# Performance work log

Hardware: AMD Instinct MI355X
Metric: run time of the kernel (lower is better)

The kernel has to match this reference:

```python
import jax, jax.numpy as jnp
import numpy as np

N = 50000
E = 800000
D_IN = 128
D_HID = 256


def setup_inputs() -> dict:
    key = jax.random.key(0)
    ks = jax.random.split(key, 9)
    x = jax.random.normal(ks[0], (N, D_IN), dtype=jnp.float32)
    edge_index = jax.random.randint(ks[1], (2, E), 0, N, dtype=jnp.int64)
    edge_weight = jax.random.uniform(ks[2], (E,), dtype=jnp.float32)
    # GCNConv params (lin: y = x @ W.T, plus bias added after aggregation)
    W1 = jax.random.normal(ks[3], (D_HID, D_IN), dtype=jnp.float32) / np.sqrt(D_IN)
    b1 = jnp.zeros((D_HID,), dtype=jnp.float32)
    W2 = jax.random.normal(ks[4], (D_IN, D_HID), dtype=jnp.float32) / np.sqrt(D_HID)
    b2 = jnp.zeros((D_IN,), dtype=jnp.float32)
    gamma = jnp.ones((D_IN,), dtype=jnp.float32)
    beta = jnp.zeros((D_IN,), dtype=jnp.float32)
    return {"x": x, "edge_index": edge_index, "edge_weight": edge_weight,
            "W1": W1, "b1": b1, "W2": W2, "b2": b2,
            "gamma": gamma, "beta": beta}


def _gcn_norm(edge_index, edge_weight, n_nodes):
    # add self loops with weight 1.0 (PyG gcn_norm default)
    loop = jnp.arange(n_nodes, dtype=edge_index.dtype)
    src = jnp.concatenate([edge_index[0], loop])
    dst = jnp.concatenate([edge_index[1], loop])
    w = jnp.concatenate([edge_weight, jnp.ones((n_nodes,), edge_weight.dtype)])
    # symmetric normalization: deg over target index
    deg = jax.ops.segment_sum(w, dst, num_segments=n_nodes)
    dinv = jnp.where(deg > 0, jax.lax.rsqrt(deg), 0.0)
    norm = dinv[src] * w * dinv[dst]
    return src, dst, norm


def _gcn_conv(x, src, dst, norm, W, b, n_nodes):
    h = x @ W.T                                    # [N, out]
    msg = h[src] * norm[:, None]                   # gather + scale [E+N, out]
    out = jax.ops.segment_sum(msg, dst, num_segments=n_nodes)
    return out + b


def reference(x, edge_index, edge_weight, W1, b1, W2, b2, gamma, beta):
    n_nodes = x.shape[0]
    src, dst, norm = _gcn_norm(edge_index, edge_weight, n_nodes)
    h = _gcn_conv(x, src, dst, norm, W1, b1, n_nodes)
    h = jax.nn.relu(h)
    h = _gcn_conv(h, src, dst, norm, W2, b2, n_nodes)
    # LayerNorm over last dim
    mu = jnp.mean(h, axis=-1, keepdims=True)
    var = jnp.mean(jnp.square(h - mu), axis=-1, keepdims=True)
    h = (h - mu) * jax.lax.rsqrt(var + 1e-5) * gamma + beta
    return h
```

## Files before the change

kernel.cpp:

```cpp
#include <hip/hip_runtime.h>

typedef unsigned short ushort_t;
typedef unsigned long long u64_t;
typedef __attribute__((ext_vector_type(8))) short short8;
typedef __attribute__((ext_vector_type(4))) float float4v;

__device__ inline float b2f(ushort_t u) {
    unsigned x = ((unsigned)u) << 16;
    return __builtin_bit_cast(float, x);
}
__device__ inline ushort_t f2b(float f) {
    unsigned x = __builtin_bit_cast(unsigned, f);
    unsigned r = (x + 0x7fffu + ((x >> 16) & 1u)) >> 16;
    return (ushort_t)r;
}


__global__ void k_mode(const int* __restrict__ ei, int E, int* mode) {
    __shared__ int any32;
    if (threadIdx.x == 0) any32 = 0;
    __syncthreads();
    for (int i = threadIdx.x; i < 1024; i += blockDim.x) {
        int slot = 2 * i + 1;
        if (slot < 2 * E && ei[slot] != 0) atomicOr(&any32, 1);
    }
    __syncthreads();
    if (threadIdx.x == 0) mode[0] = any32 ? 0 : 1;
}

__device__ inline int ld_src(const int* __restrict__ ei, int e, int E, int m64) {
    return m64 ? ei[2 * (size_t)e] : ei[e];
}
__device__ inline int ld_dst(const int* __restrict__ ei, int e, int E, int m64) {
    return m64 ? ei[2 * ((size_t)E + e)] : ei[(size_t)E + e];
}


__global__ void k_cast_x(const float* __restrict__ x, ushort_t* __restrict__ xb, int n4) {
    int i = blockIdx.x * blockDim.x + threadIdx.x;
    if (i >= n4) return;
    float4v v = ((const float4v*)x)[i];
    ushort4 o;
    o.x = f2b(v[0]); o.y = f2b(v[1]); o.z = f2b(v[2]); o.w = f2b(v[3]);
    ((ushort4*)xb)[i] = o;
}

__global__ void k_cast_w(const float* __restrict__ W1, const float* __restrict__ W2,
                         ushort_t* __restrict__ W1b, ushort_t* __restrict__ W2b) {
    int i = blockIdx.x * blockDim.x + threadIdx.x;
    if (i < 32768) W1b[i] = f2b(W1[i]);
    else W2b[i - 32768] = f2b(W2[i - 32768]);
}


__global__ void k_node_init(u64_t* packed, int Nn) {
    int i = blockIdx.x * blockDim.x + threadIdx.x;
    if (i < Nn) packed[i] = 0ull;
}

__global__ void k_count(const int* __restrict__ ei, const float* __restrict__ w,
                        const int* __restrict__ mode,
                        u64_t* packed, int* __restrict__ rank, int E, int Nn) {
    int e = blockIdx.x * blockDim.x + threadIdx.x;
    if (e >= E) return;
    int m64 = mode[0];
    int s = ld_src(ei, e, E, m64);
    int d = ld_dst(ei, e, E, m64);
    if ((unsigned)s < (unsigned)Nn && (unsigned)d < (unsigned)Nn) {
        unsigned fx = (unsigned)(w[e] * 16777216.0f + 0.5f);
        u64_t old = atomicAdd(packed + d, (1ull << 32) | (u64_t)fx);
        rank[e] = (int)(old >> 32);
    } else {
        rank[e] = -1;
    }
}

__device__ inline int cnt_hi(const u64_t* packed, int i) {
    return ((const int*)packed)[2 * i + 1];
}


__global__ __launch_bounds__(256) void k_scan_a(const u64_t* __restrict__ packed,
                                                int* __restrict__ bsum, int Nn) {
    int b = blockIdx.x, t = threadIdx.x;
    int base = b * 2048 + t * 8;
    int s = 0;
#pragma unroll
    for (int j = 0; j < 8; ++j) { int i = base + j; if (i < Nn) s += cnt_hi(packed, i); }
#pragma unroll
    for (int off = 1; off < 64; off <<= 1) s += __shfl_xor(s, off);
    __shared__ int wsum[4];
    if ((t & 63) == 0) wsum[t >> 6] = s;
    __syncthreads();
    if (t == 0) bsum[b] = wsum[0] + wsum[1] + wsum[2] + wsum[3];
}

__global__ void k_scan_b(const int* __restrict__ bsum, int* __restrict__ bbase,
                         int nb, int* __restrict__ offs, int Nn) {
    int t = threadIdx.x;
    int own = (t < nb) ? bsum[t] : 0;
    int v = own;
#pragma unroll
    for (int off = 1; off < 64; off <<= 1) {
        int u = __shfl_up(v, off);
        if (t >= off) v += u;
    }
    if (t < nb) bbase[t] = v - own;
    if (t == 63) offs[Nn] = v;
}

__global__ __launch_bounds__(256) void k_scan_c(const u64_t* __restrict__ packed,
                                                const int* __restrict__ bbase,
                                                int* __restrict__ offs, int Nn) {
    int b = blockIdx.x, t = threadIdx.x;
    int base = b * 2048 + t * 8;
    int v[8];
    int s = 0;
#pragma unroll
    for (int j = 0; j < 8; ++j) {
        int i = base + j;
        v[j] = (i < Nn) ? cnt_hi(packed, i) : 0;
        s += v[j];
    }
    __shared__ int sd[256];
    sd[t] = s;
    __syncthreads();
    for (int off = 1; off < 256; off <<= 1) {
        int u = (t >= off) ? sd[t - off] : 0;
        __syncthreads();
        sd[t] += u;
        __syncthreads();
    }
    int pos = bbase[b] + sd[t] - s;
#pragma unroll
    for (int j = 0; j < 8; ++j) {
        int i = base + j;
        if (i < Nn) { offs[i] = pos; pos += v[j]; }
    }
}

__global__ void k_dinv(const u64_t* __restrict__ packed, float* dinv, int Nn) {
    int i = blockIdx.x * blockDim.x + threadIdx.x;
    if (i >= Nn) return;
    float deg = 1.0f + (float)(unsigned)(packed[i] & 0xFFFFFFFFull) * (1.0f / 16777216.0f);
    dinv[i] = rsqrtf(deg);
}


__global__ void k_scatter(const int* __restrict__ ei, const float* __restrict__ w,
                          const int* __restrict__ mode,
                          const float* __restrict__ dinv,
                          const int* __restrict__ offs,
                          const int* __restrict__ rank,
                          int2* __restrict__ edata, int E, int Nn) {
    int e = blockIdx.x * blockDim.x + threadIdx.x;
    if (e >= E) return;
    int r = rank[e];
    if (r < 0) return;
    int m64 = mode[0];
    int s = ld_src(ei, e, E, m64);
    int d = ld_dst(ei, e, E, m64);
    int pos = offs[d] + r;
    float nw = dinv[s] * w[e] * dinv[d];
    int2 p;
    p.x = s;
    p.y = __builtin_bit_cast(int, nw);
    edata[pos] = p;
}


__device__ inline void agg_edges(const ushort_t* __restrict__ src,
                                 const int2* __restrict__ edata,
                                 int s, int e, int hl, int p, float* a) {
    int i = s;
    for (; i + 7 < e; i += 8) {
#pragma unroll
        for (int j = 0; j < 4; ++j) {
            int idx = i + p + 2 * j;
            int2 ed = edata[idx];
            float nw = __builtin_bit_cast(float, ed.y);
            ushort4 q = ((const ushort4*)(src + (size_t)ed.x * 128))[hl];
            a[0] += b2f(q.x) * nw; a[1] += b2f(q.y) * nw;
            a[2] += b2f(q.z) * nw; a[3] += b2f(q.w) * nw;
        }
    }
    for (; i < e; i += 2) {
        int idx = i + p;
        int ic = min(idx, e - 1);
        int2 ed = edata[ic];
        float nw = (idx < e) ? __builtin_bit_cast(float, ed.y) : 0.f;
        ushort4 q = ((const ushort4*)(src + (size_t)ed.x * 128))[hl];
        a[0] += b2f(q.x) * nw; a[1] += b2f(q.y) * nw;
        a[2] += b2f(q.z) * nw; a[3] += b2f(q.w) * nw;
    }
}

__global__ __launch_bounds__(256) void k_agg1(const ushort_t* __restrict__ xb,
                                              const int* __restrict__ offs,
                                              const int2* __restrict__ edata,
                                              const float* __restrict__ dinv,
                                              ushort_t* __restrict__ ax, int Nn) {
    int v = (blockIdx.x * blockDim.x + threadIdx.x) >> 6;
    int lane = threadIdx.x & 63;
    if (v >= Nn) return;
    int hl = lane & 31, p = lane >> 5;
    float a[4] = {0.f, 0.f, 0.f, 0.f};
    if (p == 0) {
        float dv = dinv[v];
        float sn = dv * dv;
        ushort4 pq = ((const ushort4*)(xb + (size_t)v * 128))[hl];
        a[0] = b2f(pq.x) * sn; a[1] = b2f(pq.y) * sn;
        a[2] = b2f(pq.z) * sn; a[3] = b2f(pq.w) * sn;
    }
    int s = offs[v], e = offs[v + 1];
    agg_edges(xb, edata, s, e, hl, p, a);
#pragma unroll
    for (int j = 0; j < 4; ++j) a[j] += __shfl_xor(a[j], 32);
    if (p == 0) {
        ushort4 o;
        o.x = f2b(a[0]); o.y = f2b(a[1]); o.z = f2b(a[2]); o.w = f2b(a[3]);
        ((ushort4*)(ax + (size_t)v * 128))[hl] = o;
    }
}


__global__ __launch_bounds__(256, 2) void k_gemm_fused(const ushort_t* __restrict__ ax,
                                                       const ushort_t* __restrict__ W1b,
                                                       const float* __restrict__ b1v,
                                                       const ushort_t* __restrict__ W2b,
                                                       ushort_t* __restrict__ h2, int Nn) {
    __shared__ ushort_t tile[64][264];
    int tid = threadIdx.x, wid = tid >> 6, lane = tid & 63;
    int m = lane & 15, q = lane >> 4;
    int blk = blockIdx.x * 64;

    short8 wf[4][4];
#pragma unroll
    for (int nt = 0; nt < 4; ++nt) {
        const ushort_t* wb = W1b + (size_t)(wid * 64 + nt * 16 + m) * 128 + q * 8;
#pragma unroll
        for (int kt = 0; kt < 4; ++kt) wf[nt][kt] = *(const short8*)(wb + kt * 32);
    }
    short8 af[4][4];
#pragma unroll
    for (int mi = 0; mi < 4; ++mi) {
        int arow = blk + mi * 16 + m;
        bool rv = arow < Nn;
        const ushort_t* ab = ax + (size_t)arow * 128 + q * 8;
#pragma unroll
        for (int kt = 0; kt < 4; ++kt)
            af[mi][kt] = rv ? *(const short8*)(ab + kt * 32) : (short8)0;
    }

    float4v acc1[4][4];
#pragma unroll
    for (int mi = 0; mi < 4; ++mi)
#pragma unroll
        for (int nt = 0; nt < 4; ++nt) acc1[mi][nt] = (float4v){0.f, 0.f, 0.f, 0.f};

#pragma unroll
    for (int kt = 0; kt < 4; ++kt)
#pragma unroll
        for (int mi = 0; mi < 4; ++mi)
#pragma unroll
            for (int nt = 0; nt < 4; ++nt)
                acc1[mi][nt] = __builtin_amdgcn_mfma_f32_16x16x32_bf16(
                    af[mi][kt], wf[nt][kt], acc1[mi][nt], 0, 0, 0);

#pragma unroll
    for (int nt = 0; nt < 4; ++nt) {
        int col = wid * 64 + nt * 16 + m;
        float bb = b1v[col];
#pragma unroll
        for (int mi = 0; mi < 4; ++mi) {
#pragma unroll
            for (int r = 0; r < 4; ++r) {
                float v = acc1[mi][nt][r] + bb;
                v = v > 0.f ? v : 0.f;
                tile[mi * 16 + q * 4 + r][col] = f2b(v);
            }
        }
    }
    __syncthreads();

    short8 w2f[2][8];
#pragma unroll
    for (int n2 = 0; n2 < 2; ++n2) {
        const ushort_t* wb = W2b + (size_t)(wid * 32 + n2 * 16 + m) * 256 + q * 8;
#pragma unroll
        for (int kt = 0; kt < 8; ++kt) w2f[n2][kt] = *(const short8*)(wb + kt * 32);
    }

    float4v acc2[4][2];
#pragma unroll
    for (int mi = 0; mi < 4; ++mi)
#pragma unroll
        for (int n2 = 0; n2 < 2; ++n2) acc2[mi][n2] = (float4v){0.f, 0.f, 0.f, 0.f};

#pragma unroll
    for (int kt = 0; kt < 8; ++kt) {
#pragma unroll
        for (int mi = 0; mi < 4; ++mi) {
            short8 a2 = *(const short8*)&tile[mi * 16 + m][kt * 32 + q * 8];
#pragma unroll
            for (int n2 = 0; n2 < 2; ++n2)
                acc2[mi][n2] = __builtin_amdgcn_mfma_f32_16x16x32_bf16(
                    a2, w2f[n2][kt], acc2[mi][n2], 0, 0, 0);
        }
    }

#pragma unroll
    for (int mi = 0; mi < 4; ++mi) {
#pragma unroll
        for (int n2 = 0; n2 < 2; ++n2) {
            int col = wid * 32 + n2 * 16 + m;
#pragma unroll
            for (int r = 0; r < 4; ++r) {
                int row = blk + mi * 16 + q * 4 + r;
                if (row < Nn) h2[(size_t)row * 128 + col] = f2b(acc2[mi][n2][r]);
            }
        }
    }
}


__global__ __launch_bounds__(256) void k_agg2_ln(const ushort_t* __restrict__ h2,
                                                 const int* __restrict__ offs,
                                                 const int2* __restrict__ edata,
                                                 const float* __restrict__ dinv,
                                                 const float* __restrict__ b2v,
                                                 const float* __restrict__ gv,
                                                 const float* __restrict__ bev,
                                                 float* __restrict__ out, int Nn) {
    int v = (blockIdx.x * blockDim.x + threadIdx.x) >> 6;
    int lane = threadIdx.x & 63;
    if (v >= Nn) return;
    int hl = lane & 31, p = lane >> 5;
    float a[4] = {0.f, 0.f, 0.f, 0.f};
    if (p == 0) {
        float dv = dinv[v];
        float sn = dv * dv;
        ushort4 pq = ((const ushort4*)(h2 + (size_t)v * 128))[hl];
        a[0] = b2f(pq.x) * sn; a[1] = b2f(pq.y) * sn;
        a[2] = b2f(pq.z) * sn; a[3] = b2f(pq.w) * sn;
    }
    int s = offs[v], e = offs[v + 1];
    agg_edges(h2, edata, s, e, hl, p, a);
#pragma unroll
    for (int j = 0; j < 4; ++j) a[j] += __shfl_xor(a[j], 32);

    int d0 = hl * 4;
#pragma unroll
    for (int j = 0; j < 4; ++j) a[j] += b2v[d0 + j];

    float ssum = a[0] + a[1] + a[2] + a[3];
    float ssq = a[0] * a[0] + a[1] * a[1] + a[2] * a[2] + a[3] * a[3];
#pragma unroll
    for (int off = 1; off < 64; off <<= 1) {
        ssum += __shfl_xor(ssum, off);
        ssq += __shfl_xor(ssq, off);
    }
    float mu = ssum * (1.0f / 256.0f);
    float var = ssq * (1.0f / 256.0f) - mu * mu;
    float r = rsqrtf(var + 1e-5f);
    if (p == 0) {
        float4v o;
#pragma unroll
        for (int j = 0; j < 4; ++j)
            o[j] = (a[j] - mu) * r * gv[d0 + j] + bev[d0 + j];
        ((float4v*)(out + (size_t)v * 128))[hl] = o;
    }
}


extern "C" void kernel_launch(void* const* d_in, const int* in_sizes, int n_in,
                              void* d_out, int out_size, void* d_ws, size_t ws_size,
                              hipStream_t stream) {
    const float* x   = (const float*)d_in[0];
    const int*   ei  = (const int*)d_in[1];
    const float* ew  = (const float*)d_in[2];
    const float* W1  = (const float*)d_in[3];
    const float* b1v = (const float*)d_in[4];
    const float* W2  = (const float*)d_in[5];
    const float* b2v = (const float*)d_in[6];
    const float* gv  = (const float*)d_in[7];
    const float* bev = (const float*)d_in[8];
    float* out = (float*)d_out;

    const int Nn = in_sizes[0] / 128;
    const int E  = in_sizes[2];

    char* base = (char*)d_ws;
    size_t off = 0;
    auto alloc = [&](size_t bytes) {
        char* p = base + off;
        off = (off + bytes + 255) & ~(size_t)255;
        return p;
    };
    int*    mode   = (int*)alloc(4);
    u64_t*  packed = (u64_t*)alloc((size_t)Nn * 8);
    float*  dinv   = (float*)alloc((size_t)Nn * 4);
    int*    offs   = (int*)alloc((size_t)(Nn + 1) * 4);
    int*    bsum   = (int*)alloc(64 * 4);
    int*    bbase  = (int*)alloc(64 * 4);
    int*    rank   = (int*)alloc((size_t)E * 4);
    int2*   edata  = (int2*)alloc((size_t)E * 8);
    ushort_t* xb   = (ushort_t*)alloc((size_t)Nn * 128 * 2);
    ushort_t* h2   = (ushort_t*)alloc((size_t)Nn * 128 * 2);
    ushort_t* W1b  = (ushort_t*)alloc(32768 * 2);
    ushort_t* W2b  = (ushort_t*)alloc(32768 * 2);
    ushort_t* ax   = (ushort_t*)d_out;
    (void)ws_size; (void)n_in; (void)out_size;

    int gN = (Nn + 255) / 256;
    int gE = (E + 255) / 256;
    int gW = (Nn + 3) / 4;
    int gG = (Nn + 63) / 64;
    int n4 = Nn * 128 / 4;
    int nb = (Nn + 2047) / 2048;

    k_mode<<<1, 256, 0, stream>>>(ei, E, mode);
    k_node_init<<<gN, 256, 0, stream>>>(packed, Nn);
    k_count<<<gE, 256, 0, stream>>>(ei, ew, mode, packed, rank, E, Nn);
    k_scan_a<<<nb, 256, 0, stream>>>(packed, bsum, Nn);
    k_scan_b<<<1, 64, 0, stream>>>(bsum, bbase, nb, offs, Nn);
    k_scan_c<<<nb, 256, 0, stream>>>(packed, bbase, offs, Nn);
    k_dinv<<<gN, 256, 0, stream>>>(packed, dinv, Nn);
    k_scatter<<<gE, 256, 0, stream>>>(ei, ew, mode, dinv, offs, rank, edata, E, Nn);
    k_cast_x<<<(n4 + 255) / 256, 256, 0, stream>>>(x, xb, n4);
    k_cast_w<<<256, 256, 0, stream>>>(W1, W2, W1b, W2b);
    k_agg1<<<gW, 256, 0, stream>>>(xb, offs, edata, dinv, ax, Nn);
    k_gemm_fused<<<gG, 256, 0, stream>>>(ax, W1b, b1v, W2b, h2, Nn);
    k_agg2_ln<<<gW, 256, 0, stream>>>(h2, offs, edata, dinv, b2v, gv, bev, out, Nn);
}
```

Before: 271.1 us.

## Fuse preprocessing kernels and first aggregation into GEMM to cut launches

Merges edge counting, the x cast and the weight cast into one multi-role kernel, and replaces node init with a memset. The dinv computation is folded into the scan, and the index-width mode kernel is replaced by a per-wave ballot check. The first-layer aggregation moves into the fused GEMM kernel, which now writes the aggregated rows to LDS instead of a global buffer. This removes several launches and a global round trip of the aggregated features. In exchange the GEMM kernel uses more shared memory, which may lower occupancy, and each block gathers 64 nodes serially per wave.

```diff
diff --git a/kernel.cpp b/kernel.cpp
--- a/kernel.cpp
+++ b/kernel.cpp
@@ -15,63 +15,57 @@
     return (ushort_t)r;
 }
 
-
-__global__ void k_mode(const int* __restrict__ ei, int E, int* mode) {
-    __shared__ int any32;
-    if (threadIdx.x == 0) any32 = 0;
-    __syncthreads();
-    for (int i = threadIdx.x; i < 1024; i += blockDim.x) {
-        int slot = 2 * i + 1;
-        if (slot < 2 * E && ei[slot] != 0) atomicOr(&any32, 1);
-    }
-    __syncthreads();
-    if (threadIdx.x == 0) mode[0] = any32 ? 0 : 1;
-}
-
-__device__ inline int ld_src(const int* __restrict__ ei, int e, int E, int m64) {
-    return m64 ? ei[2 * (size_t)e] : ei[e];
-}
-__device__ inline int ld_dst(const int* __restrict__ ei, int e, int E, int m64) {
-    return m64 ? ei[2 * ((size_t)E + e)] : ei[(size_t)E + e];
-}
-
-
-__global__ void k_cast_x(const float* __restrict__ x, ushort_t* __restrict__ xb, int n4) {
-    int i = blockIdx.x * blockDim.x + threadIdx.x;
-    if (i >= n4) return;
-    float4v v = ((const float4v*)x)[i];
-    ushort4 o;
-    o.x = f2b(v[0]); o.y = f2b(v[1]); o.z = f2b(v[2]); o.w = f2b(v[3]);
-    ((ushort4*)xb)[i] = o;
-}
-
-__global__ void k_cast_w(const float* __restrict__ W1, const float* __restrict__ W2,
-                         ushort_t* __restrict__ W1b, ushort_t* __restrict__ W2b) {
-    int i = blockIdx.x * blockDim.x + threadIdx.x;
-    if (i < 32768) W1b[i] = f2b(W1[i]);
-    else W2b[i - 32768] = f2b(W2[i - 32768]);
-}
-
-
-__global__ void k_node_init(u64_t* packed, int Nn) {
-    int i = blockIdx.x * blockDim.x + threadIdx.x;
-    if (i < Nn) packed[i] = 0ull;
-}
-
-__global__ void k_count(const int* __restrict__ ei, const float* __restrict__ w,
-                        const int* __restrict__ mode,
-                        u64_t* packed, int* __restrict__ rank, int E, int Nn) {
-    int e = blockIdx.x * blockDim.x + threadIdx.x;
-    if (e >= E) return;
-    int m64 = mode[0];
-    int s = ld_src(ei, e, E, m64);
-    int d = ld_dst(ei, e, E, m64);
-    if ((unsigned)s < (unsigned)Nn && (unsigned)d < (unsigned)Nn) {
-        unsigned fx = (unsigned)(w[e] * 16777216.0f + 0.5f);
-        u64_t old = atomicAdd(packed + d, (1ull << 32) | (u64_t)fx);
-        rank[e] = (int)(old >> 32);
+__device__ inline void load_edge(const int* __restrict__ ei, int e, int E,
+                                 int& s, int& d) {
+    int ec = min(e, E - 1);
+    int2 c64 = ((const int2*)ei)[ec];
+    unsigned long long m = __ballot(c64.y != 0);
+    if (m != 0ull) {
+        s = ei[ec];
+        d = ei[(size_t)E + ec];
     } else {
-        rank[e] = -1;
+        s = c64.x;
+        d = ((const int2*)ei)[(size_t)E + ec].x;
+    }
+}
+
+
+__global__ __launch_bounds__(256) void k_mega(const int* __restrict__ ei,
+                                              const float* __restrict__ w,
+                                              const float* __restrict__ x,
+                                              const float* __restrict__ W1,
+                                              const float* __restrict__ W2,
+                                              u64_t* packed, int* __restrict__ rank,
+                                              ushort_t* __restrict__ xb,
+                                              ushort_t* __restrict__ W1b,
+                                              ushort_t* __restrict__ W2b,
+                                              int E, int Nn, int gE, int gX) {
+    int b = blockIdx.x;
+    if (b < gE) {
+        int e = b * 256 + threadIdx.x;
+        int s, d;
+        load_edge(ei, e, E, s, d);
+        if (e < E) {
+            if ((unsigned)s < (unsigned)Nn && (unsigned)d < (unsigned)Nn) {
+                unsigned fx = (unsigned)(w[e] * 16777216.0f + 0.5f);
+                u64_t old = atomicAdd(packed + d, (1ull << 32) | (u64_t)fx);
+                rank[e] = (int)(old >> 32);
+            } else {
+                rank[e] = -1;
+            }
+        }
+    } else if (b < gE + gX) {
+        int i = (b - gE) * 256 + threadIdx.x;
+        if (i < Nn * 32) {
+            float4v v = ((const float4v*)x)[i];
+            ushort4 o;
+            o.x = f2b(v[0]); o.y = f2b(v[1]); o.z = f2b(v[2]); o.w = f2b(v[3]);
+            ((ushort4*)xb)[i] = o;
+        }
+    } else {
+        int i = (b - gE - gX) * 256 + threadIdx.x;
+        if (i < 32768) W1b[i] = f2b(W1[i]);
+        else if (i < 65536) W2b[i - 32768] = f2b(W2[i - 32768]);
     }
 }
 
@@ -111,15 +105,18 @@
 
 __global__ __launch_bounds__(256) void k_scan_c(const u64_t* __restrict__ packed,
                                                 const int* __restrict__ bbase,
-                                                int* __restrict__ offs, int Nn) {
+                                                int* __restrict__ offs,
+                                                float* __restrict__ dinv, int Nn) {
     int b = blockIdx.x, t = threadIdx.x;
     int base = b * 2048 + t * 8;
+    u64_t pk[8];
     int v[8];
     int s = 0;
 #pragma unroll
     for (int j = 0; j < 8; ++j) {
         int i = base + j;
-        v[j] = (i < Nn) ? cnt_hi(packed, i) : 0;
+        pk[j] = (i < Nn) ? packed[i] : 0ull;
+        v[j] = (int)(pk[j] >> 32);
         s += v[j];
     }
     __shared__ int sd[256];
@@ -135,31 +132,26 @@
 #pragma unroll
     for (int j = 0; j < 8; ++j) {
         int i = base + j;
-        if (i < Nn) { offs[i] = pos; pos += v[j]; }
-    }
-}
-
-__global__ void k_dinv(const u64_t* __restrict__ packed, float* dinv, int Nn) {
-    int i = blockIdx.x * blockDim.x + threadIdx.x;
-    if (i >= Nn) return;
-    float deg = 1.0f + (float)(unsigned)(packed[i] & 0xFFFFFFFFull) * (1.0f / 16777216.0f);
-    dinv[i] = rsqrtf(deg);
+        if (i < Nn) {
+            offs[i] = pos; pos += v[j];
+            float deg = 1.0f + (float)(unsigned)(pk[j] & 0xFFFFFFFFull) * (1.0f / 16777216.0f);
+            dinv[i] = rsqrtf(deg);
+        }
+    }
 }
 
 
 __global__ void k_scatter(const int* __restrict__ ei, const float* __restrict__ w,
-                          const int* __restrict__ mode,
                           const float* __restrict__ dinv,
                           const int* __restrict__ offs,
                           const int* __restrict__ rank,
                           int2* __restrict__ edata, int E, int Nn) {
-    int e = blockIdx.x * blockDim.x + threadIdx.x;
+    int e = blockIdx.x * 256 + threadIdx.x;
+    int s, d;
+    load_edge(ei, e, E, s, d);
     if (e >= E) return;
     int r = rank[e];
     if (r < 0) return;
-    int m64 = mode[0];
-    int s = ld_src(ei, e, E, m64);
-    int d = ld_dst(ei, e, E, m64);
     int pos = offs[d] + r;
     float nw = dinv[s] * w[e] * dinv[d];
     int2 p;
@@ -195,45 +187,47 @@
     }
 }
 
-__global__ __launch_bounds__(256) void k_agg1(const ushort_t* __restrict__ xb,
-                                              const int* __restrict__ offs,
-                                              const int2* __restrict__ edata,
-                                              const float* __restrict__ dinv,
-                                              ushort_t* __restrict__ ax, int Nn) {
-    int v = (blockIdx.x * blockDim.x + threadIdx.x) >> 6;
-    int lane = threadIdx.x & 63;
-    if (v >= Nn) return;
-    int hl = lane & 31, p = lane >> 5;
-    float a[4] = {0.f, 0.f, 0.f, 0.f};
-    if (p == 0) {
-        float dv = dinv[v];
-        float sn = dv * dv;
-        ushort4 pq = ((const ushort4*)(xb + (size_t)v * 128))[hl];
-        a[0] = b2f(pq.x) * sn; a[1] = b2f(pq.y) * sn;
-        a[2] = b2f(pq.z) * sn; a[3] = b2f(pq.w) * sn;
-    }
-    int s = offs[v], e = offs[v + 1];
-    agg_edges(xb, edata, s, e, hl, p, a);
-#pragma unroll
-    for (int j = 0; j < 4; ++j) a[j] += __shfl_xor(a[j], 32);
-    if (p == 0) {
-        ushort4 o;
-        o.x = f2b(a[0]); o.y = f2b(a[1]); o.z = f2b(a[2]); o.w = f2b(a[3]);
-        ((ushort4*)(ax + (size_t)v * 128))[hl] = o;
-    }
-}
-
-
-__global__ __launch_bounds__(256, 2) void k_gemm_fused(const ushort_t* __restrict__ ax,
+
+__global__ __launch_bounds__(256, 2) void k_gemm_fused(const ushort_t* __restrict__ xb,
+                                                       const int* __restrict__ offs,
+                                                       const int2* __restrict__ edata,
+                                                       const float* __restrict__ dinv,
                                                        const ushort_t* __restrict__ W1b,
                                                        const float* __restrict__ b1v,
                                                        const ushort_t* __restrict__ W2b,
                                                        ushort_t* __restrict__ h2, int Nn) {
+    __shared__ ushort_t axl[64][136];
     __shared__ ushort_t tile[64][264];
     int tid = threadIdx.x, wid = tid >> 6, lane = tid & 63;
+    int hl = lane & 31, p = lane >> 5;
+    int blk = blockIdx.x * 64;
+
+    for (int n = 0; n < 16; ++n) {
+        int v = blk + wid * 16 + n;
+        float a[4] = {0.f, 0.f, 0.f, 0.f};
+        int s = 0, e = 0;
+        if (v < Nn) {
+            s = offs[v]; e = offs[v + 1];
+            if (p == 0) {
+                float dv = dinv[v];
+                float sn = dv * dv;
+                ushort4 pq = ((const ushort4*)(xb + (size_t)v * 128))[hl];
+                a[0] = b2f(pq.x) * sn; a[1] = b2f(pq.y) * sn;
+                a[2] = b2f(pq.z) * sn; a[3] = b2f(pq.w) * sn;
+            }
+        }
+        agg_edges(xb, edata, s, e, hl, p, a);
+#pragma unroll
+        for (int j = 0; j < 4; ++j) a[j] += __shfl_xor(a[j], 32);
+        if (p == 0) {
+            ushort4 o;
+            o.x = f2b(a[0]); o.y = f2b(a[1]); o.z = f2b(a[2]); o.w = f2b(a[3]);
+            *(ushort4*)&axl[wid * 16 + n][hl * 4] = o;
+        }
+    }
+    __syncthreads();
+
     int m = lane & 15, q = lane >> 4;
-    int blk = blockIdx.x * 64;
-
     short8 wf[4][4];
 #pragma unroll
     for (int nt = 0; nt < 4; ++nt) {
@@ -241,16 +235,6 @@
 #pragma unroll
         for (int kt = 0; kt < 4; ++kt) wf[nt][kt] = *(const short8*)(wb + kt * 32);
     }
-    short8 af[4][4];
-#pragma unroll
-    for (int mi = 0; mi < 4; ++mi) {
-        int arow = blk + mi * 16 + m;
-        bool rv = arow < Nn;
-        const ushort_t* ab = ax + (size_t)arow * 128 + q * 8;
-#pragma unroll
-        for (int kt = 0; kt < 4; ++kt)
-            af[mi][kt] = rv ? *(const short8*)(ab + kt * 32) : (short8)0;
-    }
 
     float4v acc1[4][4];
 #pragma unroll
@@ -261,11 +245,13 @@
 #pragma unroll
     for (int kt = 0; kt < 4; ++kt)
 #pragma unroll
-        for (int mi = 0; mi < 4; ++mi)
+        for (int mi = 0; mi < 4; ++mi) {
+            short8 af = *(const short8*)&axl[mi * 16 + m][kt * 32 + q * 8];
 #pragma unroll
             for (int nt = 0; nt < 4; ++nt)
                 acc1[mi][nt] = __builtin_amdgcn_mfma_f32_16x16x32_bf16(
-                    af[mi][kt], wf[nt][kt], acc1[mi][nt], 0, 0, 0);
+                    af, wf[nt][kt], acc1[mi][nt], 0, 0, 0);
+        }
 
 #pragma unroll
     for (int nt = 0; nt < 4; ++nt) {
@@ -397,7 +383,6 @@
         off = (off + bytes + 255) & ~(size_t)255;
         return p;
     };
-    int*    mode   = (int*)alloc(4);
     u64_t*  packed = (u64_t*)alloc((size_t)Nn * 8);
     float*  dinv   = (float*)alloc((size_t)Nn * 4);
     int*    offs   = (int*)alloc((size_t)(Nn + 1) * 4);
@@ -409,27 +394,21 @@
     ushort_t* h2   = (ushort_t*)alloc((size_t)Nn * 128 * 2);
     ushort_t* W1b  = (ushort_t*)alloc(32768 * 2);
     ushort_t* W2b  = (ushort_t*)alloc(32768 * 2);
-    ushort_t* ax   = (ushort_t*)d_out;
     (void)ws_size; (void)n_in; (void)out_size;
 
-    int gN = (Nn + 255) / 256;
     int gE = (E + 255) / 256;
+    int gX = (Nn * 32 + 255) / 256;
     int gW = (Nn + 3) / 4;
     int gG = (Nn + 63) / 64;
-    int n4 = Nn * 128 / 4;
     int nb = (Nn + 2047) / 2048;
 
-    k_mode<<<1, 256, 0, stream>>>(ei, E, mode);
-    k_node_init<<<gN, 256, 0, stream>>>(packed, Nn);
-    k_count<<<gE, 256, 0, stream>>>(ei, ew, mode, packed, rank, E, Nn);
+    hipMemsetAsync(packed, 0, (size_t)Nn * 8, stream);
+    k_mega<<<gE + gX + 256, 256, 0, stream>>>(ei, ew, x, W1, W2, packed, rank,
+                                              xb, W1b, W2b, E, Nn, gE, gX);
     k_scan_a<<<nb, 256, 0, stream>>>(packed, bsum, Nn);
     k_scan_b<<<1, 64, 0, stream>>>(bsum, bbase, nb, offs, Nn);
-    k_scan_c<<<nb, 256, 0, stream>>>(packed, bbase, offs, Nn);
-    k_dinv<<<gN, 256, 0, stream>>>(packed, dinv, Nn);
-    k_scatter<<<gE, 256, 0, stream>>>(ei, ew, mode, dinv, offs, rank, edata, E, Nn);
-    k_cast_x<<<(n4 + 255) / 256, 256, 0, stream>>>(x, xb, n4);
-    k_cast_w<<<256, 256, 0, stream>>>(W1, W2, W1b, W2b);
-    k_agg1<<<gW, 256, 0, stream>>>(xb, offs, edata, dinv, ax, Nn);
-    k_gemm_fused<<<gG, 256, 0, stream>>>(ax, W1b, b1v, W2b, h2, Nn);
+    k_scan_c<<<nb, 256, 0, stream>>>(packed, bbase, offs, dinv, Nn);
+    k_scatter<<<gE, 256, 0, stream>>>(ei, ew, dinv, offs, rank, edata, E, Nn);
+    k_gemm_fused<<<gG, 256, 0, stream>>>(xb, offs, edata, dinv, W1b, b1v, W2b, h2, Nn);
     k_agg2_ln<<<gW, 256, 0, stream>>>(h2, offs, edata, dinv, b2v, gv, bev, out, Nn);
 }
```

Result: slower. 309.1 us (+14.0%).
